# Optimization experiments

Hardware: AMD Instinct MI355X
Metric: run time of the kernel (lower is better)

The kernel has to match this reference:

```python
import jax, jax.numpy as jnp
import numpy as np

B, T, D = 4, 2048, 1024

def layer_norm(x, gamma, bias):
    # NOTE: faithfully reproduces the source's (buggy) LN: x - mu/sqrt(var), unbiased var
    mu = jnp.mean(x, axis=-1, keepdims=True)
    var = jnp.var(x, axis=-1, ddof=1, keepdims=True)
    return (x - mu / jnp.sqrt(var)) * gamma + bias

def setup_inputs() -> dict:
    key = jax.random.key(0)
    ks = jax.random.split(key, 8)
    scale = 1.0 / np.sqrt(D)
    return {
        'x': jax.random.normal(ks[0], (B, T, D), dtype=jnp.float32),
        'gamma1': jnp.ones((D,), jnp.float32),
        'beta1': jnp.zeros((D,), jnp.float32),
        'w_q': jax.random.uniform(ks[1], (D, D), jnp.float32, -scale, scale),
        'w_k': jax.random.uniform(ks[2], (D, D), jnp.float32, -scale, scale),
        'w_v': jax.random.uniform(ks[3], (D, D), jnp.float32, -scale, scale),
        'gamma2': jnp.ones((D,), jnp.float32),
        'beta2': jnp.zeros((D,), jnp.float32),
        'W1': jax.random.uniform(ks[4], (D, D), jnp.float32, -scale, scale),
        'b1': jnp.zeros((D,), jnp.float32),
        'W2': jax.random.uniform(ks[5], (D, D), jnp.float32, -scale, scale),
        'b2': jnp.zeros((D,), jnp.float32),
    }

def reference(x, gamma1, beta1, w_q, w_k, w_v, gamma2, beta2, W1, b1, W2, b2):
    d_model = x.shape[-1]
    t = x.shape[1]
    h = layer_norm(x, gamma1, beta1)
    q = jnp.einsum('btk,kd->btd', h, w_q)
    k = jnp.einsum('btk,kd->btd', h, w_k)
    v = jnp.einsum('btk,kd->btd', h, w_v)
    scale = 1.0 / jnp.sqrt(jnp.asarray(d_model, x.dtype))
    causal = jnp.tril(jnp.ones((t, t), dtype=bool))
    mask = jnp.where(causal, 0.0, -jnp.inf).astype(x.dtype)
    scores = jnp.einsum('bqd,bkd->bqk', q, k) * scale + mask
    attn = jax.nn.softmax(scores, axis=-1)
    y = jnp.einsum('bqt,btd->bqd', attn, v) + x
    h2 = layer_norm(y, gamma2, beta2)
    out = jnp.maximum(h2 @ W1 + b1, 0.0) @ W2 + b2
    return out + y
```

## Files before the change

### kernel.cpp

```cpp
#include <hip/hip_runtime.h>
#include <hip/hip_bf16.h>
#include <math.h>

using bf16 = __hip_bfloat16;

static constexpr int Bn = 4;
static constexpr int Tn = 2048;
static constexpr int Dn = 1024;

typedef __attribute__((ext_vector_type(8))) short bf16x8;
typedef __attribute__((ext_vector_type(4))) float f32x4;

__device__ __forceinline__ float ldf(float v) { return v; }
__device__ __forceinline__ float ldf(bf16 v) { return __bfloat162float(v); }
__device__ __forceinline__ bf16 f2b(float v) { return __float2bfloat16(v); }
__device__ __forceinline__ float b2f(short s) {
    return __uint_as_float(((unsigned)(unsigned short)s) << 16);
}
__device__ __forceinline__ short f2bs(float v) {
    bf16 t = __float2bfloat16(v);
    return *reinterpret_cast<short*>(&t);
}

template <typename T> __device__ __forceinline__ T from_float(float v);
template <> __device__ __forceinline__ float from_float<float>(float v) { return v; }
template <> __device__ __forceinline__ bf16 from_float<bf16>(float v) { return f2b(v); }

__device__ __forceinline__ void load4(const float* p, float* v) {
    const float4 t = *(const float4*)p;
    v[0] = t.x; v[1] = t.y; v[2] = t.z; v[3] = t.w;
}
__device__ __forceinline__ void load4(const bf16* p, float* v) {
    const short4 t = *(const short4*)p;
    v[0] = b2f(t.x); v[1] = b2f(t.y); v[2] = b2f(t.z); v[3] = b2f(t.w);
}

__device__ __forceinline__ void async_copy16(const bf16* g, bf16* l) {
    __builtin_amdgcn_global_load_lds(
        (const __attribute__((address_space(1))) void*)g,
        (__attribute__((address_space(3))) void*)l,
        16, 0, 0);
}

template <int BM, int BN, int MINW, int EPI, typename OutT, typename ResT, bool RELU>
__global__ __launch_bounds__(256, MINW) void gemm_nt(
    const bf16* __restrict__ A, const bf16* __restrict__ Bm,
    OutT* __restrict__ C, const float* __restrict__ bias,
    const ResT* __restrict__ res, bf16* __restrict__ vtp,
    int M, int N, int K, int lda, int ldb, int ldc,
    long sA, long sB, long sC, long sR, int mode)
{
    const int bm = blockIdx.y, bn = blockIdx.x, bz = blockIdx.z;
    if (mode == 1 && bn * BN > bm * BM + (BM - 1)) return;
    const int kend = bm * BM + BM;
    const int kmax = (mode == 2) ? (kend < K ? kend : K) : K;

    const bf16* Ab = A + (size_t)bz * sA;
    const bf16* Bb = Bm + (size_t)bz * sB;

    constexpr int WROWS = BM / 64;
    constexpr int WCOLS = 4 / WROWS;
    constexpr int TM = 64;
    constexpr int TN = BN / WCOLS;
    constexpr int MT = TM / 16;
    constexpr int NT = TN / 16;
    constexpr int nA = BM / 16;
    constexpr int nB = BN / 16;
    constexpr int TSTR = 132;
    constexpr int SME = (EPI == 1) ? (BM * TSTR) : (2 * (BM + BN) * 32);

    __shared__ __align__(16) bf16 smem[SME];
    __shared__ float rs[(EPI == 3) ? BM : 1];
    bf16* As = smem;
    bf16* Bs = smem + 2 * BM * 32;

    const int tid = threadIdx.x;
    const int wave = tid >> 6;
    const int lane = tid & 63;
    const int wm = wave / WCOLS;
    const int wn = wave % WCOLS;

    f32x4 acc[MT][NT] = {};
    float rsum[MT] = {};

    const int lr = lane >> 2;
    const int lc = (lane & 3) * 8;
    const bf16* gAc[nA / 4]; bf16* lAc[nA / 4];
    const bf16* gBc[nB / 4]; bf16* lBc[nB / 4];
#pragma unroll
    for (int i = 0; i < nA / 4; ++i) {
        const int c = wave + 4 * i;
        gAc[i] = Ab + (size_t)(bm * BM + c * 16 + lr) * lda + lc;
        lAc[i] = &As[c * 512];
    }
#pragma unroll
    for (int i = 0; i < nB / 4; ++i) {
        const int c = wave + 4 * i;
        gBc[i] = Bb + (size_t)(bn * BN + c * 16 + lr) * ldb + lc;
        lBc[i] = &Bs[c * 512];
    }

    const int arow = lane & 15;
    const int kq = (lane >> 4) * 8;

    for (int k0 = 0; k0 < kmax; k0 += 64) {
#pragma unroll
        for (int hh = 0; hh < 2; ++hh) {
#pragma unroll
            for (int i = 0; i < nA / 4; ++i)
                async_copy16(gAc[i] + k0 + 32 * hh, lAc[i] + hh * (BM * 32));
#pragma unroll
            for (int i = 0; i < nB / 4; ++i)
                async_copy16(gBc[i] + k0 + 32 * hh, lBc[i] + hh * (BN * 32));
        }
        __syncthreads();

#pragma unroll
        for (int hh = 0; hh < 2; ++hh) {
            const bf16* Ah = As + hh * (BM * 32);
            const bf16* Bh = Bs + hh * (BN * 32);
            bf16x8 af[MT], bfm[NT];
#pragma unroll
            for (int t = 0; t < MT; ++t)
                af[t] = *(const bf16x8*)&Ah[(wm * TM + t * 16 + arow) * 32 + kq];
#pragma unroll
            for (int t = 0; t < NT; ++t)
                bfm[t] = *(const bf16x8*)&Bh[(wn * TN + t * 16 + arow) * 32 + kq];
            if (EPI == 3 && wn == 0) {
#pragma unroll
                for (int t = 0; t < MT; ++t)
#pragma unroll
                    for (int e = 0; e < 8; ++e) rsum[t] += b2f(af[t][e]);
            }
#pragma unroll
            for (int mt = 0; mt < MT; ++mt)
#pragma unroll
                for (int nt = 0; nt < NT; ++nt)
                    acc[mt][nt] = __builtin_amdgcn_mfma_f32_16x16x32_bf16(
                        af[mt], bfm[nt], acc[mt][nt], 0, 0, 0);
        }
        __syncthreads();
    }

    const int rowBase = bm * BM + wm * TM;
    const int colBase = bn * BN + wn * TN;
    const int qrow = (lane >> 4) * 4;
    const int ccol = lane & 15;

    if (EPI == 3) {
#pragma unroll
        for (int t = 0; t < MT; ++t) {
            float v = rsum[t];
            v += __shfl_xor(v, 16);
            v += __shfl_xor(v, 32);
            if (wn == 0 && lane < 16) rs[wm * TM + t * 16 + lane] = v;
        }
        __syncthreads();
    }

    if (EPI == 1 && bn * BN >= 2048) {
        bf16* tt = smem;
#pragma unroll
        for (int mt = 0; mt < MT; ++mt) {
            const int tl = wm * TM + mt * 16 + qrow;
#pragma unroll
            for (int nt = 0; nt < NT; ++nt) {
                const int dl = wn * TN + nt * 16 + ccol;
                short4 o;
                o.x = f2bs(acc[mt][nt][0]);
                o.y = f2bs(acc[mt][nt][1]);
                o.z = f2bs(acc[mt][nt][2]);
                o.w = f2bs(acc[mt][nt][3]);
                *(short4*)&tt[dl * TSTR + tl] = o;
            }
        }
        __syncthreads();
        const int dl = tid >> 1;
        const int th = (tid & 1) * 64;
        const int dg = bn * BN - 2048 + dl;
        const int b = (bm * BM) >> 11;
        const int tin = (bm * BM) & (Tn - 1);
        bf16* dst = vtp + ((size_t)b * Dn + dg) * Tn + tin + th;
        const bf16* srcl = &tt[dl * TSTR + th];
#pragma unroll
        for (int i = 0; i < 16; ++i)
            ((short4*)dst)[i] = ((const short4*)srcl)[i];
        return;
    }

    if (EPI == 2) {
        OutT* Cb = C + (size_t)bz * sC;
        const float scale = 0.03125f;
#pragma unroll
        for (int mt = 0; mt < MT; ++mt) {
#pragma unroll
            for (int nt = 0; nt < NT; ++nt) {
                const int cc = colBase + nt * 16 + ccol;
#pragma unroll
                for (int r = 0; r < 4; ++r) {
                    const int rr = rowBase + mt * 16 + qrow + r;
                    const float e = (cc <= rr) ? __expf(acc[mt][nt][r] * scale) : 0.0f;
                    Cb[(size_t)rr * ldc + cc] = from_float<OutT>(e);
                }
            }
        }
        return;
    }

    OutT* Cb = C + (size_t)bz * sC;
    const ResT* Rb = res ? (res + (size_t)bz * sR) : nullptr;
#pragma unroll
    for (int mt = 0; mt < MT; ++mt) {
        float inv4[4];
        if (EPI == 3) {
#pragma unroll
            for (int r = 0; r < 4; ++r)
                inv4[r] = 1.0f / rs[wm * TM + mt * 16 + qrow + r];
        }
#pragma unroll
        for (int nt = 0; nt < NT; ++nt) {
            const int cc = colBase + nt * 16 + ccol;
            const float bv = bias ? bias[cc] : 0.0f;
#pragma unroll
            for (int r = 0; r < 4; ++r) {
                const int rr = rowBase + mt * 16 + qrow + r;
                float v = acc[mt][nt][r];
                if (EPI == 3) v *= inv4[r];
                v += bv;
                if (RELU) v = fmaxf(v, 0.0f);
                if (Rb) v += ldf(Rb[(size_t)rr * ldc + cc]);
                Cb[(size_t)rr * ldc + cc] = from_float<OutT>(v);
            }
        }
    }
}

template <typename InT>
__global__ __launch_bounds__(256) void ln_kernel(
    const InT* __restrict__ x, const float* __restrict__ gamma,
    const float* __restrict__ beta, bf16* __restrict__ out)
{
    const int row = blockIdx.x;
    const int tid = threadIdx.x;
    const int j = tid * 4;
    const InT* xr = x + (size_t)row * Dn;

    float v[4];
    load4(xr + j, v);
    float s = v[0] + v[1] + v[2] + v[3];
    float sq = v[0] * v[0] + v[1] * v[1] + v[2] * v[2] + v[3] * v[3];
#pragma unroll
    for (int o = 32; o > 0; o >>= 1) {
        s += __shfl_down(s, o);
        sq += __shfl_down(sq, o);
    }
    __shared__ float red[2][4];
    const int lane = tid & 63, w = tid >> 6;
    if (lane == 0) { red[0][w] = s; red[1][w] = sq; }
    __syncthreads();
    s  = red[0][0] + red[0][1] + red[0][2] + red[0][3];
    sq = red[1][0] + red[1][1] + red[1][2] + red[1][3];
    const float mean = s / (float)Dn;
    const float var = (sq - s * s / (float)Dn) / (float)(Dn - 1);
    const float coef = mean * rsqrtf(var);

    const float4 g = *(const float4*)(gamma + j);
    const float4 be = *(const float4*)(beta + j);
    short4 o;
    o.x = f2bs((v[0] - coef) * g.x + be.x);
    o.y = f2bs((v[1] - coef) * g.y + be.y);
    o.z = f2bs((v[2] - coef) * g.z + be.z);
    o.w = f2bs((v[3] - coef) * g.w + be.w);
    *(short4*)(out + (size_t)row * Dn + j) = o;
}

struct WPtrs { const float* p[5]; };

__global__ __launch_bounds__(256) void wtrans_kernel(WPtrs wp, bf16* __restrict__ dst)
{
    __shared__ bf16 tile[32][33];
    const int z = blockIdx.z;
    const float* src = wp.p[z];
    bf16* d = dst + (size_t)z * Dn * Dn;
    const int c0 = blockIdx.x * 32, r0 = blockIdx.y * 32;
    const int tx = threadIdx.x & 31;
    const int ty = threadIdx.x >> 5;
#pragma unroll
    for (int dy = 0; dy < 32; dy += 8)
        tile[ty + dy][tx] = f2b(src[(size_t)(r0 + ty + dy) * Dn + (c0 + tx)]);
    __syncthreads();
#pragma unroll
    for (int dy = 0; dy < 32; dy += 8)
        d[(size_t)(c0 + ty + dy) * Dn + (r0 + tx)] = tile[tx][ty + dy];
}

extern "C" void kernel_launch(void* const* d_in, const int* in_sizes, int n_in,
                              void* d_out, int out_size, void* d_ws, size_t ws_size,
                              hipStream_t stream) {
    const float* x      = (const float*)d_in[0];
    const float* gamma1 = (const float*)d_in[1];
    const float* beta1  = (const float*)d_in[2];
    const float* w_q    = (const float*)d_in[3];
    const float* w_k    = (const float*)d_in[4];
    const float* w_v    = (const float*)d_in[5];
    const float* gamma2 = (const float*)d_in[6];
    const float* beta2  = (const float*)d_in[7];
    const float* W1     = (const float*)d_in[8];
    const float* b1     = (const float*)d_in[9];
    const float* W2     = (const float*)d_in[10];
    const float* b2     = (const float*)d_in[11];
    float* out = (float*)d_out;

    char* ws = (char*)d_ws;
    size_t off = 0;
    auto alloc = [&](size_t bytes) {
        char* p = ws + off;
        off += (bytes + 255) & ~(size_t)255;
        return p;
    };
    const size_t BT = (size_t)Bn * Tn;
    bf16* h    = (bf16*)alloc(BT * Dn * 2);
    bf16* qk   = (bf16*)alloc(BT * 2 * Dn * 2);
    bf16* vt   = (bf16*)alloc(BT * Dn * 2);
    bf16* wbuf = (bf16*)alloc((size_t)5 * Dn * Dn * 2);
    bf16* S    = (bf16*)alloc((size_t)Bn * Tn * Tn * 2);
    bf16* y    = (bf16*)alloc(BT * Dn * 2);
    bf16* h2   = h;
    bf16* mid  = qk;

    const dim3 blk(256);
    const long TD  = (long)Tn * Dn;
    const long TT  = (long)Tn * Tn;
    const long TD2 = (long)Tn * 2 * Dn;

    WPtrs wp; wp.p[0] = w_q; wp.p[1] = w_k; wp.p[2] = w_v; wp.p[3] = W1; wp.p[4] = W2;
    wtrans_kernel<<<dim3(32, 32, 5), blk, 0, stream>>>(wp, wbuf);

    ln_kernel<float><<<dim3((unsigned)BT), blk, 0, stream>>>(x, gamma1, beta1, h);

    gemm_nt<128, 128, 4, 1, bf16, float, false><<<dim3(24, 64, 1), blk, 0, stream>>>(
        h, wbuf, qk, nullptr, nullptr, vt,
        (int)BT, 3 * Dn, Dn, Dn, Dn, 2 * Dn, 0, 0, 0, 0, 0);

    gemm_nt<128, 128, 4, 2, bf16, float, false><<<dim3(16, 16, Bn), blk, 0, stream>>>(
        qk, qk + 1024, S, nullptr, nullptr, nullptr,
        Tn, Tn, Dn, 2 * Dn, 2 * Dn, Tn, TD2, TD2, TT, 0, 1);

    gemm_nt<128, 128, 4, 3, bf16, float, false><<<dim3(8, 16, Bn), blk, 0, stream>>>(
        S, vt, y, nullptr, x, nullptr,
        Tn, Dn, Tn, Tn, Tn, Dn, TT, TD, TD, TD, 2);

    ln_kernel<bf16><<<dim3((unsigned)BT), blk, 0, stream>>>(y, gamma2, beta2, h2);

    gemm_nt<128, 128, 4, 0, bf16, float, true><<<dim3(8, 64, 1), blk, 0, stream>>>(
        h2, wbuf + (size_t)3 * Dn * Dn, mid, b1, nullptr, nullptr,
        (int)BT, Dn, Dn, Dn, Dn, Dn, 0, 0, 0, 0, 0);

    gemm_nt<128, 128, 4, 0, float, bf16, false><<<dim3(8, 64, 1), blk, 0, stream>>>(
        mid, wbuf + (size_t)4 * Dn * Dn, out, b2, y, nullptr,
        (int)BT, Dn, Dn, Dn, Dn, Dn, 0, 0, 0, 0, 0);
}
```

Baseline: 363.5 us.

## Compute softmax row sums in score epilogue and fuse prep kernels

Softmax row sums are now accumulated with atomics in the score-GEMM epilogue, using the bf16-rounded exp values. Previously the PV GEMM summed the A-fragments inside its inner loop, and that work is removed. The weight transpose, rowsum zeroing and first layernorm are merged into one prep launch. The grid is also swapped so blockIdx.x walks M tiles, which changes the tile ordering for L2 reuse. The cost is atomic traffic and an extra global buffer read in the PV epilogue.

```diff
diff --git a/kernel.cpp b/kernel.cpp
--- a/kernel.cpp
+++ b/kernel.cpp
@@ -47,10 +47,11 @@
     const bf16* __restrict__ A, const bf16* __restrict__ Bm,
     OutT* __restrict__ C, const float* __restrict__ bias,
     const ResT* __restrict__ res, bf16* __restrict__ vtp,
+    float* __restrict__ rowsum,
     int M, int N, int K, int lda, int ldb, int ldc,
     long sA, long sB, long sC, long sR, int mode)
 {
-    const int bm = blockIdx.y, bn = blockIdx.x, bz = blockIdx.z;
+    const int bm = blockIdx.x, bn = blockIdx.y, bz = blockIdx.z;
     if (mode == 1 && bn * BN > bm * BM + (BM - 1)) return;
     const int kend = bm * BM + BM;
     const int kmax = (mode == 2) ? (kend < K ? kend : K) : K;
@@ -67,10 +68,10 @@
     constexpr int nA = BM / 16;
     constexpr int nB = BN / 16;
     constexpr int TSTR = 132;
-    constexpr int SME = (EPI == 1) ? (BM * TSTR) : (2 * (BM + BN) * 32);
+    constexpr int STAGE = 2 * (BM + BN) * 32;
+    constexpr int SME = (EPI == 1 && BM * TSTR > STAGE) ? BM * TSTR : STAGE;
 
     __shared__ __align__(16) bf16 smem[SME];
-    __shared__ float rs[(EPI == 3) ? BM : 1];
     bf16* As = smem;
     bf16* Bs = smem + 2 * BM * 32;
 
@@ -81,7 +82,6 @@
     const int wn = wave % WCOLS;
 
     f32x4 acc[MT][NT] = {};
-    float rsum[MT] = {};
 
     const int lr = lane >> 2;
     const int lc = (lane & 3) * 8;
@@ -126,12 +126,6 @@
 #pragma unroll
             for (int t = 0; t < NT; ++t)
                 bfm[t] = *(const bf16x8*)&Bh[(wn * TN + t * 16 + arow) * 32 + kq];
-            if (EPI == 3 && wn == 0) {
-#pragma unroll
-                for (int t = 0; t < MT; ++t)
-#pragma unroll
-                    for (int e = 0; e < 8; ++e) rsum[t] += b2f(af[t][e]);
-            }
 #pragma unroll
             for (int mt = 0; mt < MT; ++mt)
 #pragma unroll
@@ -146,17 +140,6 @@
     const int colBase = bn * BN + wn * TN;
     const int qrow = (lane >> 4) * 4;
     const int ccol = lane & 15;
-
-    if (EPI == 3) {
-#pragma unroll
-        for (int t = 0; t < MT; ++t) {
-            float v = rsum[t];
-            v += __shfl_xor(v, 16);
-            v += __shfl_xor(v, 32);
-            if (wn == 0 && lane < 16) rs[wm * TM + t * 16 + lane] = v;
-        }
-        __syncthreads();
-    }
 
     if (EPI == 1 && bn * BN >= 2048) {
         bf16* tt = smem;
@@ -190,32 +173,52 @@
 
     if (EPI == 2) {
         OutT* Cb = C + (size_t)bz * sC;
+        float* rsb = rowsum + (size_t)bz * Tn;
         const float scale = 0.03125f;
 #pragma unroll
         for (int mt = 0; mt < MT; ++mt) {
+            float rsv[4] = {0.f, 0.f, 0.f, 0.f};
 #pragma unroll
             for (int nt = 0; nt < NT; ++nt) {
                 const int cc = colBase + nt * 16 + ccol;
 #pragma unroll
                 for (int r = 0; r < 4; ++r) {
                     const int rr = rowBase + mt * 16 + qrow + r;
-                    const float e = (cc <= rr) ? __expf(acc[mt][nt][r] * scale) : 0.0f;
-                    Cb[(size_t)rr * ldc + cc] = from_float<OutT>(e);
+                    float e = 0.0f;
+                    if (cc <= rr) {
+                        const short es = f2bs(__expf(acc[mt][nt][r] * scale));
+                        Cb[(size_t)rr * ldc + cc] = *(const bf16*)&es;
+                        e = b2f(es);
+                    } else {
+                        Cb[(size_t)rr * ldc + cc] = from_float<OutT>(0.0f);
+                    }
+                    rsv[r] += e;
                 }
             }
+#pragma unroll
+            for (int r = 0; r < 4; ++r) {
+                float v = rsv[r];
+                v += __shfl_xor(v, 1);
+                v += __shfl_xor(v, 2);
+                v += __shfl_xor(v, 4);
+                v += __shfl_xor(v, 8);
+                if (ccol == 0)
+                    atomicAdd(rsb + rowBase + mt * 16 + qrow + r, v);
+            }
         }
         return;
     }
 
     OutT* Cb = C + (size_t)bz * sC;
     const ResT* Rb = res ? (res + (size_t)bz * sR) : nullptr;
+    const float* rsb = (EPI == 3) ? (rowsum + (size_t)bz * Tn) : nullptr;
 #pragma unroll
     for (int mt = 0; mt < MT; ++mt) {
         float inv4[4];
         if (EPI == 3) {
 #pragma unroll
             for (int r = 0; r < 4; ++r)
-                inv4[r] = 1.0f / rs[wm * TM + mt * 16 + qrow + r];
+                inv4[r] = 1.0f / rsb[rowBase + mt * 16 + qrow + r];
         }
 #pragma unroll
         for (int nt = 0; nt < NT; ++nt) {
@@ -236,15 +239,11 @@
 }
 
 template <typename InT>
-__global__ __launch_bounds__(256) void ln_kernel(
-    const InT* __restrict__ x, const float* __restrict__ gamma,
-    const float* __restrict__ beta, bf16* __restrict__ out)
+__device__ __forceinline__ void ln_row(
+    const InT* __restrict__ xr, const float* __restrict__ gamma,
+    const float* __restrict__ beta, bf16* __restrict__ orow, int tid)
 {
-    const int row = blockIdx.x;
-    const int tid = threadIdx.x;
     const int j = tid * 4;
-    const InT* xr = x + (size_t)row * Dn;
-
     float v[4];
     load4(xr + j, v);
     float s = v[0] + v[1] + v[2] + v[3];
@@ -271,27 +270,52 @@
     o.y = f2bs((v[1] - coef) * g.y + be.y);
     o.z = f2bs((v[2] - coef) * g.z + be.z);
     o.w = f2bs((v[3] - coef) * g.w + be.w);
-    *(short4*)(out + (size_t)row * Dn + j) = o;
+    *(short4*)(orow + j) = o;
+}
+
+template <typename InT>
+__global__ __launch_bounds__(256) void ln_kernel(
+    const InT* __restrict__ x, const float* __restrict__ gamma,
+    const float* __restrict__ beta, bf16* __restrict__ out)
+{
+    const int row = blockIdx.x;
+    ln_row(x + (size_t)row * Dn, gamma, beta, out + (size_t)row * Dn, threadIdx.x);
 }
 
 struct WPtrs { const float* p[5]; };
 
-__global__ __launch_bounds__(256) void wtrans_kernel(WPtrs wp, bf16* __restrict__ dst)
+__global__ __launch_bounds__(256) void prep_kernel(
+    WPtrs wp, bf16* __restrict__ wdst, float* __restrict__ rowsum,
+    const float* __restrict__ x, const float* __restrict__ gamma1,
+    const float* __restrict__ beta1, bf16* __restrict__ h)
 {
-    __shared__ bf16 tile[32][33];
-    const int z = blockIdx.z;
-    const float* src = wp.p[z];
-    bf16* d = dst + (size_t)z * Dn * Dn;
-    const int c0 = blockIdx.x * 32, r0 = blockIdx.y * 32;
-    const int tx = threadIdx.x & 31;
-    const int ty = threadIdx.x >> 5;
-#pragma unroll
-    for (int dy = 0; dy < 32; dy += 8)
-        tile[ty + dy][tx] = f2b(src[(size_t)(r0 + ty + dy) * Dn + (c0 + tx)]);
-    __syncthreads();
-#pragma unroll
-    for (int dy = 0; dy < 32; dy += 8)
-        d[(size_t)(c0 + ty + dy) * Dn + (r0 + tx)] = tile[tx][ty + dy];
+    const int bx = blockIdx.x;
+    if (bx < 5120) {
+        __shared__ bf16 tile[32][33];
+        const int z = bx >> 10;
+        const int t = bx & 1023;
+        const float* src = wp.p[z];
+        bf16* d = wdst + (size_t)z * Dn * Dn;
+        const int c0 = (t & 31) * 32, r0 = (t >> 5) * 32;
+        const int tx = threadIdx.x & 31;
+        const int ty = threadIdx.x >> 5;
+#pragma unroll
+        for (int dy = 0; dy < 32; dy += 8)
+            tile[ty + dy][tx] = f2b(src[(size_t)(r0 + ty + dy) * Dn + (c0 + tx)]);
+        __syncthreads();
+#pragma unroll
+        for (int dy = 0; dy < 32; dy += 8)
+            d[(size_t)(c0 + ty + dy) * Dn + (r0 + tx)] = tile[tx][ty + dy];
+    } else if (bx < 5128) {
+        const int idx = (bx - 5120) * 1024 + (int)threadIdx.x;
+        const int base = (bx - 5120) * 1024;
+#pragma unroll
+        for (int i = 0; i < 4; ++i) rowsum[base + i * 256 + threadIdx.x] = 0.0f;
+        (void)idx;
+    } else {
+        const int row = bx - 5128;
+        ln_row(x + (size_t)row * Dn, gamma1, beta1, h + (size_t)row * Dn, threadIdx.x);
+    }
 }
 
 extern "C" void kernel_launch(void* const* d_in, const int* in_sizes, int n_in,
@@ -325,6 +349,7 @@
     bf16* wbuf = (bf16*)alloc((size_t)5 * Dn * Dn * 2);
     bf16* S    = (bf16*)alloc((size_t)Bn * Tn * Tn * 2);
     bf16* y    = (bf16*)alloc(BT * Dn * 2);
+    float* rowsum = (float*)alloc((size_t)Bn * Tn * 4);
     bf16* h2   = h;
     bf16* mid  = qk;
 
@@ -334,29 +359,28 @@
     const long TD2 = (long)Tn * 2 * Dn;
 
     WPtrs wp; wp.p[0] = w_q; wp.p[1] = w_k; wp.p[2] = w_v; wp.p[3] = W1; wp.p[4] = W2;
-    wtrans_kernel<<<dim3(32, 32, 5), blk, 0, stream>>>(wp, wbuf);
-
-    ln_kernel<float><<<dim3((unsigned)BT), blk, 0, stream>>>(x, gamma1, beta1, h);
-
-    gemm_nt<128, 128, 4, 1, bf16, float, false><<<dim3(24, 64, 1), blk, 0, stream>>>(
-        h, wbuf, qk, nullptr, nullptr, vt,
+    prep_kernel<<<dim3(5128 + (unsigned)BT, 1, 1), blk, 0, stream>>>(
+        wp, wbuf, rowsum, x, gamma1, beta1, h);
+
+    gemm_nt<128, 128, 4, 1, bf16, float, false><<<dim3(64, 24, 1), blk, 0, stream>>>(
+        h, wbuf, qk, nullptr, nullptr, vt, nullptr,
         (int)BT, 3 * Dn, Dn, Dn, Dn, 2 * Dn, 0, 0, 0, 0, 0);
 
     gemm_nt<128, 128, 4, 2, bf16, float, false><<<dim3(16, 16, Bn), blk, 0, stream>>>(
-        qk, qk + 1024, S, nullptr, nullptr, nullptr,
+        qk, qk + 1024, S, nullptr, nullptr, nullptr, rowsum,
         Tn, Tn, Dn, 2 * Dn, 2 * Dn, Tn, TD2, TD2, TT, 0, 1);
 
-    gemm_nt<128, 128, 4, 3, bf16, float, false><<<dim3(8, 16, Bn), blk, 0, stream>>>(
-        S, vt, y, nullptr, x, nullptr,
+    gemm_nt<128, 128, 4, 3, bf16, float, false><<<dim3(16, 8, Bn), blk, 0, stream>>>(
+        S, vt, y, nullptr, x, nullptr, rowsum,
         Tn, Dn, Tn, Tn, Tn, Dn, TT, TD, TD, TD, 2);
 
     ln_kernel<bf16><<<dim3((unsigned)BT), blk, 0, stream>>>(y, gamma2, beta2, h2);
 
-    gemm_nt<128, 128, 4, 0, bf16, float, true><<<dim3(8, 64, 1), blk, 0, stream>>>(
-        h2, wbuf + (size_t)3 * Dn * Dn, mid, b1, nullptr, nullptr,
+    gemm_nt<128, 128, 4, 0, bf16, float, true><<<dim3(64, 8, 1), blk, 0, stream>>>(
+        h2, wbuf + (size_t)3 * Dn * Dn, mid, b1, nullptr, nullptr, nullptr,
         (int)BT, Dn, Dn, Dn, Dn, Dn, 0, 0, 0, 0, 0);
 
-    gemm_nt<128, 128, 4, 0, float, bf16, false><<<dim3(8, 64, 1), blk, 0, stream>>>(
-        mid, wbuf + (size_t)4 * Dn * Dn, out, b2, y, nullptr,
+    gemm_nt<128, 128, 4, 0, float, bf16, false><<<dim3(64, 8, 1), blk, 0, stream>>>(
+        mid, wbuf + (size_t)4 * Dn * Dn, out, b2, y, nullptr, nullptr,
         (int)BT, Dn, Dn, Dn, Dn, Dn, 0, 0, 0, 0, 0);
 }
```

Result: faster. 348.3 us (-4.2%).
